# Optimization experiments

Measured on AMD Instinct MI355X. Metric: run time of the kernel, lower is better.

The kernel has to match this reference:

```python
import jax, jax.numpy as jnp
import numpy as np

RADII = {1: 0.031, 2: 0.028, 3: 0.128, 4: 0.096, 5: 0.084, 6: 0.073, 7: 0.071, 8: 0.066, 9: 0.057, 10: 0.058, 11: 0.166, 12: 0.141, 13: 0.121, 14: 0.111, 15: 0.107, 16: 0.105, 17: 0.102, 18: 0.106, 19: 0.2029, 20: 0.176, 21: 0.17, 22: 0.16, 23: 0.153, 24: 0.139, 25: 0.15, 26: 0.142, 27: 0.138, 28: 0.124, 29: 0.132, 30: 0.122, 31: 0.122, 32: 0.12, 33: 0.119, 34: 0.12, 35: 0.12, 36: 0.116, 37: 0.22, 38: 0.195, 39: 0.19, 40: 0.175, 41: 0.164, 42: 0.154, 43: 0.147, 44: 0.146, 45: 0.142, 46: 0.139, 47: 0.145, 48: 0.144, 49: 0.142, 50: 0.139, 51: 0.139, 52: 0.138, 53: 0.139, 54: 0.14, 55: 0.244, 56: 0.215, 57: 0.207, 58: 0.204, 59: 0.2029, 60: 0.2009, 61: 0.199, 62: 0.198, 63: 0.198, 64: 0.196, 65: 0.194, 66: 0.192, 67: 0.192, 68: 0.189, 69: 0.19, 70: 0.187, 71: 0.187, 72: 0.175, 73: 0.17, 74: 0.162, 75: 0.151, 76: 0.144, 77: 0.141, 78: 0.136, 79: 0.136, 80: 0.132, 81: 0.145, 82: 0.146, 83: 0.148, 84: 0.14, 85: 0.15, 86: 0.15, 87: 0.26, 88: 0.221, 89: 0.215, 90: 0.206, 91: 0.2, 92: 0.196, 93: 0.19, 94: 0.187, 95: 0.18, 96: 0.169}

N_ATOMS = 1_000_000
N_EDGES = 16_000_000
NUM_SYSTEMS = 10_000
MAX_Z = 97  # atomic numbers 1..96 valid
COULOMB = 138.9354576   # kJ/mol * nm / e^2
A_PREF = 0.8854 * 0.0529177210903  # Bohr-radius prefactor in nm


def setup_inputs() -> dict:
    key = jax.random.key(0)
    k1, k2, k3, k4 = jax.random.split(key, 4)
    local_pair_indices = jax.random.randint(k1, (2, N_EDGES), 0, N_ATOMS)
    # positive distances in nm, safely away from zero
    local_d_ij = jax.random.uniform(k2, (N_EDGES,), jnp.float32, 0.01, 0.5)
    atomic_numbers = jax.random.randint(k3, (N_ATOMS,), 1, MAX_Z)
    atomic_subsystem_indices = jnp.sort(
        jax.random.randint(k4, (N_ATOMS,), 0, NUM_SYSTEMS))
    radii_table = np.zeros(MAX_Z, dtype=np.float32)
    for z, r in RADII.items():
        radii_table[z] = r
    return {
        'local_d_ij': local_d_ij,
        'radii_table': jnp.asarray(radii_table),
        'local_pair_indices': local_pair_indices,
        'atomic_numbers': atomic_numbers,
        'atomic_subsystem_indices': atomic_subsystem_indices,
    }


def reference(local_d_ij, radii_table, local_pair_indices, atomic_numbers,
              atomic_subsystem_indices):
    idx_i = local_pair_indices[0]
    idx_j = local_pair_indices[1]
    # torch filters edges by idx_i < idx_j (data-dependent shape); here we
    # keep fixed shapes and zero masked contributions -> identical sums.
    mask = idx_i < idx_j

    zi_int = atomic_numbers[idx_i]
    zj_int = atomic_numbers[idx_j]
    zi = zi_int.astype(jnp.float32)
    zj = zj_int.astype(jnp.float32)
    ri = radii_table[zi_int]
    rj = radii_table[zj_int]

    d_ij = local_d_ij
    a = A_PREF / (zi ** 0.23 + zj ** 0.23)
    d = d_ij / a
    f = (0.1818 * jnp.exp(-3.2 * d)
         + 0.5099 * jnp.exp(-0.9423 * d)
         + 0.2802 * jnp.exp(-0.4029 * d)
         + 0.02817 * jnp.exp(-0.2016 * d))
    rsum = ri + rj
    phi = jnp.where(d_ij < rsum,
                    0.5 * (jnp.cos(jnp.pi * d_ij / rsum) + 1.0),
                    0.0)
    energy = f * phi * COULOMB * zi * zj / d_ij
    energy = jnp.where(mask, energy, 0.0)

    seg = atomic_subsystem_indices[idx_i]
    per_system = jax.ops.segment_sum(energy, seg, num_segments=NUM_SYSTEMS)
    return per_system.reshape(-1, 1)
```

## Files before the change

kernel.cpp:

```cpp
#include <hip/hip_runtime.h>


constexpr int MAXZ = 97;
constexpr int NBINS_PAD = 10240;
constexpr int NREP = 512;
constexpr int NPART = 32;

constexpr double LOG2E_D = 1.4426950408889634;
constexpr float A_INV = (float)(1.0 / (0.8854 * 0.0529177210903));
constexpr float C1 = (float)(-3.2    * LOG2E_D);
constexpr float C2 = (float)(-0.9423 * LOG2E_D);
constexpr float C3 = (float)(-0.4029 * LOG2E_D);
constexpr float C4 = (float)(-0.2016 * LOG2E_D);
constexpr float COUL = 138.9354576f;
constexpr float RMAX = 0.26f;

typedef int   iv4 __attribute__((ext_vector_type(4)));
typedef float fv4 __attribute__((ext_vector_type(4)));
typedef float fv2 __attribute__((ext_vector_type(2)));

__global__ void zero_kernel(float* __restrict__ out, int n) {
    int i = blockIdx.x * blockDim.x + threadIdx.x;
    if (i < n) out[i] = 0.0f;
}

__global__ void pack_kernel(const int* __restrict__ z,
                            const int* __restrict__ seg,
                            unsigned int* __restrict__ packed, int n) {
    int i = blockIdx.x * blockDim.x + threadIdx.x;
    if (i < n)
        packed[i] = (unsigned int)z[i] | ((unsigned int)seg[i] << 8);
}

__device__ __forceinline__ float zbl_energy(int zi, int zj, float d,
                                            const fv2* s_rz, bool& pass) {
    fv2 rzi = s_rz[zi];
    fv2 rzj = s_rz[zj];
    float rsum = rzi.x + rzj.x;
    pass = (d < rsum);
    float dA = d * (rzi.y + rzj.y) * A_INV;
    float f = 0.1818f  * __builtin_exp2f(C1 * dA)
            + 0.5099f  * __builtin_exp2f(C2 * dA)
            + 0.2802f  * __builtin_exp2f(C3 * dA)
            + 0.02817f * __builtin_exp2f(C4 * dA);
    float tt = d * __builtin_amdgcn_rcpf(rsum);
    float phi = 0.5f * (__builtin_amdgcn_cosf(0.5f * tt) + 1.0f);
    return f * phi * (COUL * (float)zi * (float)zj) * __builtin_amdgcn_rcpf(d);
}


__global__ __launch_bounds__(1024)
void zbl_hist_kernel(const float* __restrict__ d_ij,
                     const float* __restrict__ radii,
                     const int* __restrict__ idx_i,
                     const int* __restrict__ idx_j,
                     const unsigned int* __restrict__ packed,
                     float* __restrict__ rep,
                     int n_edges) {
    __shared__ float s_hist[NBINS_PAD];
    __shared__ fv2 s_rz[128];
    const int t = threadIdx.x;

    for (int b = t; b < NBINS_PAD; b += 1024) s_hist[b] = 0.0f;
    if (t < 128) {
        fv2 v;
        v.x = (t < MAXZ) ? radii[t] : 0.0f;
        v.y = __builtin_exp2f(0.23f * __builtin_log2f((float)t));
        s_rz[t] = v;
    }
    __syncthreads();

    const int ngrp = n_edges >> 3;
    const int stride = gridDim.x * blockDim.x;
    for (int g = blockIdx.x * blockDim.x + t; g < ngrp; g += stride) {
        const iv4* pii = reinterpret_cast<const iv4*>(idx_i) + 2 * g;
        const iv4* pjj = reinterpret_cast<const iv4*>(idx_j) + 2 * g;
        const fv4* pdd = reinterpret_cast<const fv4*>(d_ij) + 2 * g;
        iv4 ii0 = __builtin_nontemporal_load(pii);
        iv4 ii1 = __builtin_nontemporal_load(pii + 1);
        iv4 jj0 = __builtin_nontemporal_load(pjj);
        iv4 jj1 = __builtin_nontemporal_load(pjj + 1);
        fv4 dd0 = __builtin_nontemporal_load(pdd);
        fv4 dd1 = __builtin_nontemporal_load(pdd + 1);

        int ia[8], ja[8];
        float da[8];
#pragma unroll
        for (int k = 0; k < 4; ++k) {
            ia[k] = ii0[k]; ia[4 + k] = ii1[k];
            ja[k] = jj0[k]; ja[4 + k] = jj1[k];
            da[k] = dd0[k]; da[4 + k] = dd1[k];
        }

        unsigned int pia[8];
        bool m[8];
#pragma unroll
        for (int k = 0; k < 8; ++k) {
            m[k] = ia[k] < ja[k];
            pia[k] = packed[m[k] ? ia[k] : 0];
        }

        bool need[8];
        float ri[8];
        unsigned int pja[8];
#pragma unroll
        for (int k = 0; k < 8; ++k) {
            int zi = (int)(pia[k] & 0xFFu);
            ri[k] = s_rz[zi].x;
            need[k] = m[k] && (da[k] < ri[k] + RMAX);
            pja[k] = packed[need[k] ? ja[k] : 0];
        }

#pragma unroll
        for (int k = 0; k < 8; ++k) {
            if (need[k]) {
                int zi = (int)(pia[k] & 0xFFu);
                int zj = (int)(pja[k] & 0xFFu);
                int seg = (int)(pia[k] >> 8);
                bool pass;
                float e = zbl_energy(zi, zj, da[k], s_rz, pass);
                if (pass) atomicAdd(&s_hist[seg], e);
            }
        }
    }

    if (blockIdx.x == 0 && t == 0) {
        for (int e = ngrp << 3; e < n_edges; ++e) {
            int i = idx_i[e], j = idx_j[e];
            if (i < j) {
                unsigned int pi = packed[i], pj = packed[j];
                bool pass;
                float en = zbl_energy((int)(pi & 0xFFu), (int)(pj & 0xFFu),
                                      d_ij[e], s_rz, pass);
                if (pass) atomicAdd(&s_hist[(int)(pi >> 8)], en);
            }
        }
    }

    __syncthreads();
    fv4* __restrict__ rp =
        reinterpret_cast<fv4*>(rep + (size_t)blockIdx.x * NBINS_PAD);
    const fv4* sh = reinterpret_cast<const fv4*>(s_hist);
    for (int q = t; q < NBINS_PAD / 4; q += 1024)
        rp[q] = sh[q];
}

__global__ __launch_bounds__(256)
void reduce1_kernel(const float* __restrict__ rep,
                    float* __restrict__ partial) {
    int bin = blockIdx.x * 256 + threadIdx.x;
    int s = blockIdx.y;
    float acc = 0.0f;
    for (int r = s; r < NREP; r += NPART)
        acc += rep[(size_t)r * NBINS_PAD + bin];
    partial[(size_t)s * NBINS_PAD + bin] = acc;
}

__global__ __launch_bounds__(256)
void reduce2_kernel(const float* __restrict__ partial,
                    float* __restrict__ out, int out_size) {
    int bin = blockIdx.x * 256 + threadIdx.x;
    if (bin < out_size) {
        float acc = 0.0f;
        for (int s = 0; s < NPART; ++s)
            acc += partial[(size_t)s * NBINS_PAD + bin];
        out[bin] = acc;
    }
}


template <bool PACKED>
__global__ __launch_bounds__(256)
void zbl_atomic_kernel(const float* __restrict__ d_ij,
                       const float* __restrict__ radii,
                       const int* __restrict__ idx_i,
                       const int* __restrict__ idx_j,
                       const unsigned int* __restrict__ packed,
                       const int* __restrict__ atomz,
                       const int* __restrict__ subsys,
                       float* __restrict__ out,
                       int nchunk) {
    __shared__ fv2 s_rz[128];
    int t = threadIdx.x;
    if (t < 128) {
        fv2 v;
        v.x = (t < MAXZ) ? radii[t] : 0.0f;
        v.y = __builtin_exp2f(0.23f * __builtin_log2f((float)t));
        s_rz[t] = v;
    }
    __syncthreads();

    int chunk = blockIdx.x * blockDim.x + threadIdx.x;
    if (chunk >= nchunk) return;

    iv4 ii = reinterpret_cast<const iv4*>(idx_i)[chunk];
    iv4 jj = reinterpret_cast<const iv4*>(idx_j)[chunk];
    fv4 dd = reinterpret_cast<const fv4*>(d_ij)[chunk];

#pragma unroll
    for (int k = 0; k < 4; ++k) {
        int i = ii[k];
        int j = jj[k];
        float d = dd[k];
        if (i < j) {
            int zi, zj, seg;
            if (PACKED) {
                unsigned int pi = packed[i];
                unsigned int pj = packed[j];
                zi = (int)(pi & 0xFFu);
                zj = (int)(pj & 0xFFu);
                seg = (int)(pi >> 8);
            } else {
                zi = atomz[i];
                zj = atomz[j];
                seg = subsys[i];
            }
            bool pass;
            float e = zbl_energy(zi, zj, d, s_rz, pass);
            if (pass) atomicAdd(out + seg, e);
        }
    }
}

extern "C" void kernel_launch(void* const* d_in, const int* in_sizes, int n_in,
                              void* d_out, int out_size, void* d_ws, size_t ws_size,
                              hipStream_t stream) {
    const float* d_ij  = (const float*)d_in[0];
    const float* radii = (const float*)d_in[1];
    const int* pairs   = (const int*)d_in[2];
    const int* atomz   = (const int*)d_in[3];
    const int* subsys  = (const int*)d_in[4];
    float* out = (float*)d_out;

    const int n_edges = in_sizes[2] / 2;
    const int n_atoms = in_sizes[3];
    const int* idx_i = pairs;
    const int* idx_j = pairs + n_edges;

    const size_t packed_bytes = (size_t)n_atoms * sizeof(unsigned int);
    const size_t rep_bytes = (size_t)NREP * NBINS_PAD * sizeof(float);
    const size_t part_bytes = (size_t)NPART * NBINS_PAD * sizeof(float);

    if (ws_size >= packed_bytes + rep_bytes + part_bytes) {
        unsigned int* packed = (unsigned int*)d_ws;
        float* rep = (float*)((char*)d_ws + packed_bytes);
        float* partial = (float*)((char*)d_ws + packed_bytes + rep_bytes);

        pack_kernel<<<(n_atoms + 255) / 256, 256, 0, stream>>>(atomz, subsys,
                                                               packed, n_atoms);
        zbl_hist_kernel<<<NREP, 1024, 0, stream>>>(
            d_ij, radii, idx_i, idx_j, packed, rep, n_edges);
        dim3 g1(NBINS_PAD / 256, NPART);
        reduce1_kernel<<<g1, 256, 0, stream>>>(rep, partial);
        reduce2_kernel<<<(out_size + 255) / 256, 256, 0, stream>>>(
            partial, out, out_size);
    } else {
        zero_kernel<<<(out_size + 255) / 256, 256, 0, stream>>>(out, out_size);
        const int nchunk = n_edges / 4;
        const int blocks = (nchunk + 255) / 256;
        if (ws_size >= packed_bytes) {
            unsigned int* packed = (unsigned int*)d_ws;
            pack_kernel<<<(n_atoms + 255) / 256, 256, 0, stream>>>(
                atomz, subsys, packed, n_atoms);
            zbl_atomic_kernel<true><<<blocks, 256, 0, stream>>>(
                d_ij, radii, idx_i, idx_j, packed, atomz, subsys, out, nchunk);
        } else {
            zbl_atomic_kernel<false><<<blocks, 256, 0, stream>>>(
                d_ij, radii, idx_i, idx_j, nullptr, atomz, subsys, out, nchunk);
        }
    }
}
```

Before: 310.1 us.

## Pack per-atom data into 16-bit entries with windowed segment bases; single-pass reduce

Atom data is compressed from 32-bit (z | seg<<8) to 16-bit entries holding z and a segment offset relative to a per-64-atom window base. The window bases are staged in shared memory. This halves the footprint of the random-gather table, so more of it should stay in cache. The two-stage replica reduction becomes one kernel with 8 independent accumulators, which drops a launch and the intermediate buffer. The 16-bit scheme assumes sorted subsystem indices and a segment span within 512 per window, and relies on NWIN_MAX. The single reduce kernel runs only 40 blocks, so it may lose parallelism.

```diff
diff --git a/kernel.cpp b/kernel.cpp
--- a/kernel.cpp
+++ b/kernel.cpp
@@ -5,6 +5,8 @@
 constexpr int NBINS_PAD = 10240;
 constexpr int NREP = 512;
 constexpr int NPART = 32;
+constexpr int WIN_SHIFT = 6;
+constexpr int NWIN_MAX = 15632;
 
 constexpr double LOG2E_D = 1.4426950408889634;
 constexpr float A_INV = (float)(1.0 / (0.8854 * 0.0529177210903));
@@ -22,6 +24,20 @@
 __global__ void zero_kernel(float* __restrict__ out, int n) {
     int i = blockIdx.x * blockDim.x + threadIdx.x;
     if (i < n) out[i] = 0.0f;
+}
+
+__global__ void pack16_kernel(const int* __restrict__ z,
+                              const int* __restrict__ seg,
+                              unsigned short* __restrict__ p16,
+                              unsigned short* __restrict__ segb, int n) {
+    int i = blockIdx.x * blockDim.x + threadIdx.x;
+    if (i < n) {
+        int s = seg[i];
+        int base = seg[(i >> WIN_SHIFT) << WIN_SHIFT];
+        p16[i] = (unsigned short)((unsigned)z[i] | ((unsigned)(s - base) << 7));
+        if ((i & ((1 << WIN_SHIFT) - 1)) == 0)
+            segb[i >> WIN_SHIFT] = (unsigned short)s;
+    }
 }
 
 __global__ void pack_kernel(const int* __restrict__ z,
@@ -54,14 +70,18 @@
                      const float* __restrict__ radii,
                      const int* __restrict__ idx_i,
                      const int* __restrict__ idx_j,
-                     const unsigned int* __restrict__ packed,
+                     const unsigned short* __restrict__ p16,
+                     const unsigned short* __restrict__ segb_g,
+                     int nwin,
                      float* __restrict__ rep,
                      int n_edges) {
     __shared__ float s_hist[NBINS_PAD];
     __shared__ fv2 s_rz[128];
+    __shared__ unsigned short s_segb[NWIN_MAX];
     const int t = threadIdx.x;
 
     for (int b = t; b < NBINS_PAD; b += 1024) s_hist[b] = 0.0f;
+    for (int b = t; b < nwin; b += 1024) s_segb[b] = segb_g[b];
     if (t < 128) {
         fv2 v;
         v.x = (t < MAXZ) ? radii[t] : 0.0f;
@@ -97,29 +117,31 @@
 #pragma unroll
         for (int k = 0; k < 8; ++k) {
             m[k] = ia[k] < ja[k];
-            pia[k] = packed[m[k] ? ia[k] : 0];
+            pia[k] = p16[m[k] ? ia[k] : 0];
         }
 
         bool need[8];
-        float ri[8];
         unsigned int pja[8];
 #pragma unroll
         for (int k = 0; k < 8; ++k) {
-            int zi = (int)(pia[k] & 0xFFu);
-            ri[k] = s_rz[zi].x;
-            need[k] = m[k] && (da[k] < ri[k] + RMAX);
-            pja[k] = packed[need[k] ? ja[k] : 0];
+            int zi = (int)(pia[k] & 127u);
+            float ri = s_rz[zi].x;
+            need[k] = m[k] && (da[k] < ri + RMAX);
+            pja[k] = p16[need[k] ? ja[k] : 0];
         }
 
 #pragma unroll
         for (int k = 0; k < 8; ++k) {
             if (need[k]) {
-                int zi = (int)(pia[k] & 0xFFu);
-                int zj = (int)(pja[k] & 0xFFu);
-                int seg = (int)(pia[k] >> 8);
+                int zi = (int)(pia[k] & 127u);
+                int zj = (int)(pja[k] & 127u);
                 bool pass;
                 float e = zbl_energy(zi, zj, da[k], s_rz, pass);
-                if (pass) atomicAdd(&s_hist[seg], e);
+                if (pass) {
+                    int seg = (int)s_segb[ia[k] >> WIN_SHIFT]
+                            + (int)(pia[k] >> 7);
+                    atomicAdd(&s_hist[seg], e);
+                }
             }
         }
     }
@@ -128,11 +150,14 @@
         for (int e = ngrp << 3; e < n_edges; ++e) {
             int i = idx_i[e], j = idx_j[e];
             if (i < j) {
-                unsigned int pi = packed[i], pj = packed[j];
+                unsigned int pi = p16[i], pj = p16[j];
                 bool pass;
-                float en = zbl_energy((int)(pi & 0xFFu), (int)(pj & 0xFFu),
+                float en = zbl_energy((int)(pi & 127u), (int)(pj & 127u),
                                       d_ij[e], s_rz, pass);
-                if (pass) atomicAdd(&s_hist[(int)(pi >> 8)], en);
+                if (pass) {
+                    int seg = (int)segb_g[i >> WIN_SHIFT] + (int)(pi >> 7);
+                    atomicAdd(&s_hist[seg], en);
+                }
             }
         }
     }
@@ -146,26 +171,24 @@
 }
 
 __global__ __launch_bounds__(256)
-void reduce1_kernel(const float* __restrict__ rep,
-                    float* __restrict__ partial) {
+void reduce_all_kernel(const float* __restrict__ rep,
+                       float* __restrict__ out, int out_size) {
     int bin = blockIdx.x * 256 + threadIdx.x;
-    int s = blockIdx.y;
-    float acc = 0.0f;
-    for (int r = s; r < NREP; r += NPART)
-        acc += rep[(size_t)r * NBINS_PAD + bin];
-    partial[(size_t)s * NBINS_PAD + bin] = acc;
-}
-
-__global__ __launch_bounds__(256)
-void reduce2_kernel(const float* __restrict__ partial,
-                    float* __restrict__ out, int out_size) {
-    int bin = blockIdx.x * 256 + threadIdx.x;
-    if (bin < out_size) {
-        float acc = 0.0f;
-        for (int s = 0; s < NPART; ++s)
-            acc += partial[(size_t)s * NBINS_PAD + bin];
-        out[bin] = acc;
-    }
+    const float* p = rep + bin;
+    float a0 = 0.f, a1 = 0.f, a2 = 0.f, a3 = 0.f;
+    float a4 = 0.f, a5 = 0.f, a6 = 0.f, a7 = 0.f;
+    for (int r = 0; r < NREP; r += 8) {
+        a0 += p[(size_t)(r + 0) * NBINS_PAD];
+        a1 += p[(size_t)(r + 1) * NBINS_PAD];
+        a2 += p[(size_t)(r + 2) * NBINS_PAD];
+        a3 += p[(size_t)(r + 3) * NBINS_PAD];
+        a4 += p[(size_t)(r + 4) * NBINS_PAD];
+        a5 += p[(size_t)(r + 5) * NBINS_PAD];
+        a6 += p[(size_t)(r + 6) * NBINS_PAD];
+        a7 += p[(size_t)(r + 7) * NBINS_PAD];
+    }
+    float s = ((a0 + a1) + (a2 + a3)) + ((a4 + a5) + (a6 + a7));
+    if (bin < out_size) out[bin] = s;
 }
 
 
@@ -237,23 +260,24 @@
     const int* idx_i = pairs;
     const int* idx_j = pairs + n_edges;
 
+    const int nwin = (n_atoms + (1 << WIN_SHIFT) - 1) >> WIN_SHIFT;
+    const size_t p16_bytes  = ((size_t)n_atoms * 2 + 255) & ~(size_t)255;
+    const size_t segb_bytes = ((size_t)nwin * 2 + 255) & ~(size_t)255;
+    const size_t rep_bytes  = (size_t)NREP * NBINS_PAD * sizeof(float);
     const size_t packed_bytes = (size_t)n_atoms * sizeof(unsigned int);
-    const size_t rep_bytes = (size_t)NREP * NBINS_PAD * sizeof(float);
-    const size_t part_bytes = (size_t)NPART * NBINS_PAD * sizeof(float);
-
-    if (ws_size >= packed_bytes + rep_bytes + part_bytes) {
-        unsigned int* packed = (unsigned int*)d_ws;
-        float* rep = (float*)((char*)d_ws + packed_bytes);
-        float* partial = (float*)((char*)d_ws + packed_bytes + rep_bytes);
-
-        pack_kernel<<<(n_atoms + 255) / 256, 256, 0, stream>>>(atomz, subsys,
-                                                               packed, n_atoms);
+
+    if (nwin <= NWIN_MAX &&
+        ws_size >= p16_bytes + segb_bytes + rep_bytes) {
+        unsigned short* p16  = (unsigned short*)d_ws;
+        unsigned short* segb = (unsigned short*)((char*)d_ws + p16_bytes);
+        float* rep = (float*)((char*)d_ws + p16_bytes + segb_bytes);
+
+        pack16_kernel<<<(n_atoms + 255) / 256, 256, 0, stream>>>(
+            atomz, subsys, p16, segb, n_atoms);
         zbl_hist_kernel<<<NREP, 1024, 0, stream>>>(
-            d_ij, radii, idx_i, idx_j, packed, rep, n_edges);
-        dim3 g1(NBINS_PAD / 256, NPART);
-        reduce1_kernel<<<g1, 256, 0, stream>>>(rep, partial);
-        reduce2_kernel<<<(out_size + 255) / 256, 256, 0, stream>>>(
-            partial, out, out_size);
+            d_ij, radii, idx_i, idx_j, p16, segb, nwin, rep, n_edges);
+        reduce_all_kernel<<<NBINS_PAD / 256, 256, 0, stream>>>(
+            rep, out, out_size);
     } else {
         zero_kernel<<<(out_size + 255) / 256, 256, 0, stream>>>(out, out_size);
         const int nchunk = n_edges / 4;
```

New measurement: 320.9 us. 1.03x slower.
